# Kernel tuning notes

Hardware: AMD Instinct MI355X
Metric: run time of the kernel (lower is better)

## Reference

```python
import jax, jax.numpy as jnp
import numpy as np

B, V, C = 8, 6890, 16          # meshes, verts per mesh, class channels
F = 13776                       # faces per mesh (SMPL-like)
FTOT = B * F
H, W, K = 512, 512, 1           # image size, faces per pixel


def setup_inputs() -> dict:
    key = jax.random.key(0)
    k1, k2, k3, k4 = jax.random.split(key, 4)
    # padded per-vertex class features [B, V, C]
    verts_class = jax.random.normal(k1, (B, V, C), dtype=jnp.float32)
    # packed faces: per-mesh faces index into offset (packed) vertex array
    base_faces = jax.random.randint(k2, (B, F, 3), 0, V, dtype=jnp.int32)
    offsets = (jnp.arange(B, dtype=jnp.int32) * V)[:, None, None]
    faces = (base_faces + offsets).reshape(FTOT, 3)
    # pix_to_face in [-1, FTOT); -1 marks background pixels
    pix_to_face = jax.random.randint(k3, (B, H, W, K), -1, FTOT, dtype=jnp.int32)
    # barycentric coords, normalized to sum to 1
    bary = jax.random.uniform(k4, (B, H, W, K, 3), dtype=jnp.float32) + 1e-3
    bary_coords = bary / jnp.sum(bary, axis=-1, keepdims=True)
    return {
        "verts_class": verts_class,
        "faces": faces,
        "pix_to_face": pix_to_face,
        "bary_coords": bary_coords,
    }


def reference(verts_class, faces, pix_to_face, bary_coords):
    # padded_to_packed: [B, V, C] -> [B*V, C]
    vc_packed = verts_class.reshape(-1, verts_class.shape[-1])
    # gather per-face vertex attributes: [FTOT, 3, C]
    faces_class = vc_packed[faces]
    # interpolate_face_attributes
    valid = pix_to_face >= 0                       # [B,H,W,K]
    idx = jnp.where(valid, pix_to_face, 0)
    gathered = faces_class[idx]                    # [B,H,W,K,3,C]
    seg = jnp.einsum("bhwkv,bhwkvc->bhwkc", bary_coords, gathered)
    seg = jnp.where(valid[..., None], seg, 0.0)    # zero background pixels
    seg = seg.astype(jnp.int32)                    # .long() in torch
    # segmentation_map[..., :, 0] -> take channel 0: [B,H,W,K]
    return seg[..., 0]
```

## Files before the change

kernel.cpp:

```cpp
#include <hip/hip_runtime.h>


#define VC_C 16

__global__ void gather_face_attr_kernel(const float* __restrict__ vc,
                                        const int* __restrict__ faces,
                                        float4* __restrict__ fa, int ftot) {
    int f = blockIdx.x * blockDim.x + threadIdx.x;
    if (f >= ftot) return;
    int v0 = faces[3 * f + 0];
    int v1 = faces[3 * f + 1];
    int v2 = faces[3 * f + 2];
    fa[f] = make_float4(vc[(long long)v0 * VC_C],
                        vc[(long long)v1 * VC_C],
                        vc[(long long)v2 * VC_C], 0.0f);
}

__global__ void seg_shader_kernel(const float4* __restrict__ fa,
                                  const int* __restrict__ p2f,
                                  const float* __restrict__ bary,
                                  int* __restrict__ out, int npix4) {
    int i = blockIdx.x * blockDim.x + threadIdx.x;
    if (i >= npix4) return;
    int base = i * 4;

    const int4 pf = *reinterpret_cast<const int4*>(p2f + base);
    const float4 b0 = *reinterpret_cast<const float4*>(bary + (long long)base * 3);
    const float4 b1 = *reinterpret_cast<const float4*>(bary + (long long)base * 3 + 4);
    const float4 b2 = *reinterpret_cast<const float4*>(bary + (long long)base * 3 + 8);

    float w[12] = {b0.x, b0.y, b0.z, b0.w,
                   b1.x, b1.y, b1.z, b1.w,
                   b2.x, b2.y, b2.z, b2.w};
    int pfv[4] = {pf.x, pf.y, pf.z, pf.w};
    int res[4];

#pragma unroll
    for (int j = 0; j < 4; ++j) {
        int r = 0;
        int f = pfv[j];
        if (f >= 0) {
            float4 a = fa[f];
            float s = w[3 * j + 0] * a.x + w[3 * j + 1] * a.y + w[3 * j + 2] * a.z;
            r = (int)s;
        }
        res[j] = r;
    }

    int4 o = make_int4(res[0], res[1], res[2], res[3]);
    *reinterpret_cast<int4*>(out + base) = o;
}

__global__ void seg_shader_direct_kernel(const float* __restrict__ vc,
                                         const int* __restrict__ faces,
                                         const int* __restrict__ p2f,
                                         const float* __restrict__ bary,
                                         int* __restrict__ out, int npix) {
    int i = blockIdx.x * blockDim.x + threadIdx.x;
    if (i >= npix) return;
    int f = p2f[i];
    int r = 0;
    if (f >= 0) {
        int v0 = faces[3 * f + 0];
        int v1 = faces[3 * f + 1];
        int v2 = faces[3 * f + 2];
        float w0 = bary[3 * (long long)i + 0];
        float w1 = bary[3 * (long long)i + 1];
        float w2 = bary[3 * (long long)i + 2];
        float s = w0 * vc[(long long)v0 * VC_C] +
                  w1 * vc[(long long)v1 * VC_C] +
                  w2 * vc[(long long)v2 * VC_C];
        r = (int)s;
    }
    out[i] = r;
}

extern "C" void kernel_launch(void* const* d_in, const int* in_sizes, int n_in,
                              void* d_out, int out_size, void* d_ws, size_t ws_size,
                              hipStream_t stream) {
    const float* verts_class = (const float*)d_in[0];
    const int*   faces       = (const int*)d_in[1];
    const int*   pix_to_face = (const int*)d_in[2];
    const float* bary        = (const float*)d_in[3];
    int*         out         = (int*)d_out;

    const int ftot = in_sizes[1] / 3;
    const int npix = out_size;
    const size_t fa_bytes = (size_t)ftot * sizeof(float4);

    if (d_ws != nullptr && ws_size >= fa_bytes && (npix % 4) == 0) {
        float4* fa = (float4*)d_ws;
        {
            int threads = 256;
            int blocks = (ftot + threads - 1) / threads;
            gather_face_attr_kernel<<<blocks, threads, 0, stream>>>(
                verts_class, faces, fa, ftot);
        }
        {
            int npix4 = npix / 4;
            int threads = 256;
            int blocks = (npix4 + threads - 1) / threads;
            seg_shader_kernel<<<blocks, threads, 0, stream>>>(
                fa, pix_to_face, bary, out, npix4);
        }
    } else {
        int threads = 256;
        int blocks = (npix + threads - 1) / threads;
        seg_shader_direct_kernel<<<blocks, threads, 0, stream>>>(
            verts_class, faces, pix_to_face, bary, out, npix);
    }
}
```

Baseline: 27.30 us.

## Process eight pixels per thread with nontemporal loads and batched gathers

The shader kernel now handles eight pixels per thread. Its streaming loads and stores use nontemporal builtins, and all eight face-attribute gathers are issued together, without branching, before any arithmetic. This exposes more memory-level parallelism and keeps streaming data from polluting the cache. The face gather kernel now uses one thread per face-vertex, so its reads of the faces array are coalesced, but the 4th float of each face record is no longer written. Per-thread work doubles, which raises register pressure and halves the number of threads.

```diff
diff --git a/kernel.cpp b/kernel.cpp
--- a/kernel.cpp
+++ b/kernel.cpp
@@ -3,52 +3,57 @@
 
 #define VC_C 16
 
+typedef int   vint4   __attribute__((ext_vector_type(4)));
+typedef float vfloat4 __attribute__((ext_vector_type(4)));
+
 __global__ void gather_face_attr_kernel(const float* __restrict__ vc,
                                         const int* __restrict__ faces,
-                                        float4* __restrict__ fa, int ftot) {
-    int f = blockIdx.x * blockDim.x + threadIdx.x;
-    if (f >= ftot) return;
-    int v0 = faces[3 * f + 0];
-    int v1 = faces[3 * f + 1];
-    int v2 = faces[3 * f + 2];
-    fa[f] = make_float4(vc[(long long)v0 * VC_C],
-                        vc[(long long)v1 * VC_C],
-                        vc[(long long)v2 * VC_C], 0.0f);
+                                        float* __restrict__ fa_f, int n3) {
+    int t = blockIdx.x * blockDim.x + threadIdx.x;
+    if (t >= n3) return;
+    int f = t / 3;
+    int j = t - 3 * f;
+    int v = faces[t];
+    fa_f[4 * f + j] = vc[(long long)v * VC_C];
 }
 
-__global__ void seg_shader_kernel(const float4* __restrict__ fa,
-                                  const int* __restrict__ p2f,
-                                  const float* __restrict__ bary,
-                                  int* __restrict__ out, int npix4) {
+__global__ void seg_shader_kernel(const vfloat4* __restrict__ fa,
+                                  const vint4* __restrict__ p2f4,
+                                  const vfloat4* __restrict__ bary4,
+                                  vint4* __restrict__ out4, int n8) {
     int i = blockIdx.x * blockDim.x + threadIdx.x;
-    if (i >= npix4) return;
-    int base = i * 4;
+    if (i >= n8) return;
 
-    const int4 pf = *reinterpret_cast<const int4*>(p2f + base);
-    const float4 b0 = *reinterpret_cast<const float4*>(bary + (long long)base * 3);
-    const float4 b1 = *reinterpret_cast<const float4*>(bary + (long long)base * 3 + 4);
-    const float4 b2 = *reinterpret_cast<const float4*>(bary + (long long)base * 3 + 8);
+    const vint4 pfa = __builtin_nontemporal_load(p2f4 + 2 * (long long)i);
+    const vint4 pfb = __builtin_nontemporal_load(p2f4 + 2 * (long long)i + 1);
 
-    float w[12] = {b0.x, b0.y, b0.z, b0.w,
-                   b1.x, b1.y, b1.z, b1.w,
-                   b2.x, b2.y, b2.z, b2.w};
-    int pfv[4] = {pf.x, pf.y, pf.z, pf.w};
-    int res[4];
+    vfloat4 bb[6];
+#pragma unroll
+    for (int j = 0; j < 6; ++j)
+        bb[j] = __builtin_nontemporal_load(bary4 + 6 * (long long)i + j);
+    const float* w = reinterpret_cast<const float*>(bb);
 
+    int pfv[8] = {pfa.x, pfa.y, pfa.z, pfa.w, pfb.x, pfb.y, pfb.z, pfb.w};
+
+    vfloat4 a[8];
 #pragma unroll
-    for (int j = 0; j < 4; ++j) {
-        int r = 0;
-        int f = pfv[j];
-        if (f >= 0) {
-            float4 a = fa[f];
-            float s = w[3 * j + 0] * a.x + w[3 * j + 1] * a.y + w[3 * j + 2] * a.z;
-            r = (int)s;
-        }
-        res[j] = r;
+    for (int j = 0; j < 8; ++j) {
+        int f = pfv[j] >= 0 ? pfv[j] : 0;
+        a[j] = fa[f];
     }
 
-    int4 o = make_int4(res[0], res[1], res[2], res[3]);
-    *reinterpret_cast<int4*>(out + base) = o;
+    int res[8];
+#pragma unroll
+    for (int j = 0; j < 8; ++j) {
+        float s = w[3 * j + 0] * a[j].x + w[3 * j + 1] * a[j].y +
+                  w[3 * j + 2] * a[j].z;
+        res[j] = pfv[j] >= 0 ? (int)s : 0;
+    }
+
+    vint4 o0 = {res[0], res[1], res[2], res[3]};
+    vint4 o1 = {res[4], res[5], res[6], res[7]};
+    __builtin_nontemporal_store(o0, out4 + 2 * (long long)i);
+    __builtin_nontemporal_store(o1, out4 + 2 * (long long)i + 1);
 }
 
 __global__ void seg_shader_direct_kernel(const float* __restrict__ vc,
@@ -86,22 +91,24 @@
 
     const int ftot = in_sizes[1] / 3;
     const int npix = out_size;
-    const size_t fa_bytes = (size_t)ftot * sizeof(float4);
+    const size_t fa_bytes = (size_t)ftot * 4 * sizeof(float);
 
-    if (d_ws != nullptr && ws_size >= fa_bytes && (npix % 4) == 0) {
-        float4* fa = (float4*)d_ws;
+    if (d_ws != nullptr && ws_size >= fa_bytes && (npix % 8) == 0) {
+        float* fa_f = (float*)d_ws;
         {
+            int n3 = ftot * 3;
             int threads = 256;
-            int blocks = (ftot + threads - 1) / threads;
+            int blocks = (n3 + threads - 1) / threads;
             gather_face_attr_kernel<<<blocks, threads, 0, stream>>>(
-                verts_class, faces, fa, ftot);
+                verts_class, faces, fa_f, n3);
         }
         {
-            int npix4 = npix / 4;
+            int n8 = npix / 8;
             int threads = 256;
-            int blocks = (npix4 + threads - 1) / threads;
+            int blocks = (n8 + threads - 1) / threads;
             seg_shader_kernel<<<blocks, threads, 0, stream>>>(
-                fa, pix_to_face, bary, out, npix4);
+                (const vfloat4*)d_ws, (const vint4*)pix_to_face,
+                (const vfloat4*)bary, (vint4*)out, n8);
         }
     } else {
         int threads = 256;
```

Result: slower. 34.27 us (+25.5%).
